# Kernel optimization log

Hardware: AMD Instinct MI355X
Metric: run time of the kernel (lower is better)

The kernel has to match this reference:

```python
import jax, jax.numpy as jnp
import numpy as np

FG_FRACTION = 0.5
BATCHSIZE = 256
NUM_IMAGES = 1
NUM_CLASSES = 21
FG_THRESH = 0.5
BG_THRESH_HI = 0.5
BG_THRESH_LO = 0.1
ROIS_PER_IMAGE = BATCHSIZE // NUM_IMAGES                      # 256
FG_ROIS_PER_IMAGE = int(round(FG_FRACTION * ROIS_PER_IMAGE))  # 128
BG_ROIS_PER_IMAGE = ROIS_PER_IMAGE - FG_ROIS_PER_IMAGE        # 128


def _make_boxes(key, n, img=1000.0, max_wh=200.0):
    k1, k2 = jax.random.split(key)
    xy = jax.random.uniform(k1, (n, 2), dtype=jnp.float32) * (img - max_wh)
    wh = jax.random.uniform(k2, (n, 2), dtype=jnp.float32) * max_wh + 1.0
    return jnp.concatenate([xy, xy + wh], axis=1)  # valid [x1,y1,x2,y2]


def setup_inputs() -> dict:
    key = jax.random.key(0)
    k1, k2, k3 = jax.random.split(key, 3)
    N, G = 250000, 128
    rois = _make_boxes(k1, N)
    all_rois = jnp.concatenate([jnp.zeros((N, 1), jnp.float32), rois], axis=1)  # [N,5], col0 = image idx
    gt_boxes = _make_boxes(k2, G)                                               # [G,4]
    gt_labels = jax.random.randint(k3, (G,), 1, NUM_CLASSES).astype(jnp.int32)  # fg classes 1..20
    return {"all_rois": all_rois, "gt_boxes": gt_boxes, "gt_labels": gt_labels}


def _iou(a, b):
    area_a = (a[:, 2] - a[:, 0] + 1.0) * (a[:, 3] - a[:, 1] + 1.0)
    area_b = (b[:, 2] - b[:, 0] + 1.0) * (b[:, 3] - b[:, 1] + 1.0)
    ix1 = jnp.maximum(a[:, None, 0], b[None, :, 0])
    iy1 = jnp.maximum(a[:, None, 1], b[None, :, 1])
    ix2 = jnp.minimum(a[:, None, 2], b[None, :, 2])
    iy2 = jnp.minimum(a[:, None, 3], b[None, :, 3])
    iw = jnp.clip(ix2 - ix1 + 1.0, 0.0)
    ih = jnp.clip(iy2 - iy1 + 1.0, 0.0)
    inter = iw * ih
    return inter / (area_a[:, None] + area_b[None, :] - inter)


def _bbox_transform(ex, gt):
    ew = ex[:, 2] - ex[:, 0] + 1.0
    eh = ex[:, 3] - ex[:, 1] + 1.0
    ecx = ex[:, 0] + 0.5 * ew
    ecy = ex[:, 1] + 0.5 * eh
    gw = gt[:, 2] - gt[:, 0] + 1.0
    gh = gt[:, 3] - gt[:, 1] + 1.0
    gcx = gt[:, 0] + 0.5 * gw
    gcy = gt[:, 1] + 0.5 * gh
    return jnp.stack([(gcx - ecx) / ew, (gcy - ecy) / eh,
                      jnp.log(gw / ew), jnp.log(gh / eh)], axis=1)


def _proposal_target(all_rois, gt_boxes, gt_labels):
    G = gt_boxes.shape[0]
    # append gt boxes (with image-index 0 column) to the proposal set
    gt_rois = jnp.concatenate([jnp.zeros((G, 1), all_rois.dtype), gt_boxes], axis=1)
    all_rois = jnp.concatenate([all_rois, gt_rois], axis=0)          # [N+G, 5]

    overlaps = _iou(all_rois[:, 1:5], gt_boxes)                       # [N+G, G] -- dominant memory traffic
    gt_assignment = jnp.argmax(overlaps, axis=1)                      # [N+G]
    max_ov = jnp.max(overlaps, axis=1)                                # [N+G]
    labels_all = gt_labels[gt_assignment]                             # [N+G]

    fg_mask = max_ov >= FG_THRESH
    bg_mask = (max_ov < BG_THRESH_HI) & (max_ov >= BG_THRESH_LO)

    # random fg/bg sampling: top-k over random keys restricted to each mask
    u = jax.random.uniform(jax.random.key(42), (all_rois.shape[0],), dtype=jnp.float32)
    fg_idx = jax.lax.top_k(jnp.where(fg_mask, u, -1.0), FG_ROIS_PER_IMAGE)[1]
    bg_idx = jax.lax.top_k(jnp.where(bg_mask, u, -1.0), BG_ROIS_PER_IMAGE)[1]
    keep = jnp.concatenate([fg_idx, bg_idx])                          # [256]

    valid_fg = fg_mask[fg_idx]  # if fewer fg than requested, pad slots get label 0
    labels = jnp.concatenate([jnp.where(valid_fg, labels_all[fg_idx], 0),
                              jnp.zeros((BG_ROIS_PER_IMAGE,), labels_all.dtype)])

    rois = all_rois[keep]                                             # [256, 5]
    targets = _bbox_transform(rois[:, 1:5], gt_boxes[gt_assignment[keep]])  # [256, 4]

    # scatter targets into class-specific columns [256, 4*num_classes]
    onehot = jax.nn.one_hot(labels, NUM_CLASSES, dtype=targets.dtype)
    bbox_targets = (onehot[:, :, None] * targets[:, None, :]).reshape(ROIS_PER_IMAGE, 4 * NUM_CLASSES)
    bbox_targets = bbox_targets * (labels > 0)[:, None].astype(targets.dtype)
    return rois, labels, bbox_targets


def reference(all_rois, gt_boxes, gt_labels):
    return _proposal_target(all_rois, gt_boxes, gt_labels)
```

## Files before the change

### kernel.cpp

```cpp
#include <hip/hip_runtime.h>
#include <stdint.h>

#define GMAX 128
#define TK 128
#define NBINS 4096
#define CAND_MAX 4096
#define NUM_CLASSES 21

typedef float f32x4u __attribute__((ext_vector_type(4), aligned(4)));

__device__ __forceinline__ void threefry2x32(uint32_t k0, uint32_t k1,
                                             uint32_t& x0, uint32_t& x1) {
  uint32_t ks0 = k0, ks1 = k1, ks2 = k0 ^ k1 ^ 0x1BD11BDAu;
  x0 += ks0; x1 += ks1;
#define TF_ROUND(r) { x0 += x1; x1 = (x1 << (r)) | (x1 >> (32 - (r))); x1 ^= x0; }
  TF_ROUND(13) TF_ROUND(15) TF_ROUND(26) TF_ROUND(6)
  x0 += ks1; x1 += ks2 + 1u;
  TF_ROUND(17) TF_ROUND(29) TF_ROUND(16) TF_ROUND(24)
  x0 += ks2; x1 += ks0 + 2u;
  TF_ROUND(13) TF_ROUND(15) TF_ROUND(26) TF_ROUND(6)
  x0 += ks0; x1 += ks1 + 3u;
  TF_ROUND(17) TF_ROUND(29) TF_ROUND(16) TF_ROUND(24)
  x0 += ks1; x1 += ks2 + 4u;
  TF_ROUND(13) TF_ROUND(15) TF_ROUND(26) TF_ROUND(6)
  x0 += ks2; x1 += ks0 + 5u;
#undef TF_ROUND
}

__global__ void __launch_bounds__(512)
score_kernel(const float* __restrict__ all_rois,
             const float* __restrict__ gt_boxes,
             uint32_t* __restrict__ score,
             uint32_t* __restrict__ hist,
             int* __restrict__ meta,
             int N, int M, int G) {
  __shared__ uint64_t lds_key[256];
  const int t = threadIdx.x;
  const int lane = t & 63;
  const int wave = t >> 6;
  const int wq = wave & 3;
  const int half = __builtin_amdgcn_readfirstlane(wave >> 2);
  const int i = blockIdx.x * 256 + wq * 64 + lane;
  const bool active = (i < M);

  float bx1 = 0.0f, by1 = 0.0f, bx2 = 0.0f, by2 = 0.0f;
  if (active) {
    if (i < N) {
      f32x4u v = *reinterpret_cast<const f32x4u*>(all_rois + (size_t)i * 5 + 1);
      bx1 = v.x; by1 = v.y; bx2 = v.z; by2 = v.w;
    } else {
      float4 b = reinterpret_cast<const float4*>(gt_boxes)[i - N];
      bx1 = b.x; by1 = b.y; bx2 = b.z; by2 = b.w;
    }
  }
  const float area = __fmul_rn(__fadd_rn(__fsub_rn(bx2, bx1), 1.0f),
                               __fadd_rn(__fsub_rn(by2, by1), 1.0f));
  float best = -1.0f;
  int bi = 0;
  const float4* __restrict__ gt4 = reinterpret_cast<const float4*>(gt_boxes);
  const int g0 = half * 64;
#pragma unroll 8
  for (int g = 0; g < 64; ++g) {
    const float4 gb = gt4[g0 + g];
    float ga = __fmul_rn(__fadd_rn(__fsub_rn(gb.z, gb.x), 1.0f),
                         __fadd_rn(__fsub_rn(gb.w, gb.y), 1.0f));
    float ix1 = fmaxf(bx1, gb.x);
    float iy1 = fmaxf(by1, gb.y);
    float ix2 = fminf(bx2, gb.z);
    float iy2 = fminf(by2, gb.w);
    float iw = fmaxf(__fadd_rn(__fsub_rn(ix2, ix1), 1.0f), 0.0f);
    float ih = fmaxf(__fadd_rn(__fsub_rn(iy2, iy1), 1.0f), 0.0f);
    float inter = __fmul_rn(iw, ih);
    float uni = __fsub_rn(__fadd_rn(area, ga), inter);
    float ov = __fdiv_rn(inter, uni);
    if (ov > best) { best = ov; bi = g0 + g; }
  }

  const uint64_t mykey = ((uint64_t)__float_as_uint(best) << 32) |
                         (uint64_t)(uint32_t)(127 - bi);
  if (half == 1) lds_key[wq * 64 + lane] = mykey;
  __syncthreads();

  if (half == 0) {
    uint64_t kk = lds_key[wq * 64 + lane];
    if (mykey > kk) kk = mykey;
    best = __uint_as_float((uint32_t)(kk >> 32));
    bi = 127 - (int)(kk & 127ull);

    if (active) {
      uint32_t cx0 = 0u, cx1 = (uint32_t)i;
      threefry2x32(0u, 42u, cx0, cx1);
      uint32_t ubits = (cx0 ^ cx1) >> 9;
      uint32_t fg = (best >= 0.5f) ? 1u : 0u;
      uint32_t bg = (!fg && best >= 0.1f) ? 1u : 0u;
      score[i] = (ubits << 9) | ((uint32_t)bi << 2) | (fg << 1) | bg;
      if (fg)      atomicAdd(&hist[ubits >> 11], 1u);
      else if (bg) atomicAdd(&hist[NBINS + (ubits >> 11)], 1u);
    }
  }

  asm volatile("s_waitcnt vmcnt(0)" ::: "memory");
  __syncthreads();
  __shared__ unsigned s_prev;
  if (t == 0) s_prev = atomicAdd((unsigned int*)&meta[2], 1u);
  __syncthreads();
  if (s_prev != gridDim.x - 1) return;

  __shared__ uint64_t gs[512];
  __shared__ int s_jstar[2];
  const int b0 = 8 * t;
  uint64_t acc = 0;
  for (int k = 0; k < 8; ++k) {
    uint32_t hf = __hip_atomic_load(&hist[b0 + k], __ATOMIC_RELAXED,
                                    __HIP_MEMORY_SCOPE_AGENT);
    uint32_t hb = __hip_atomic_load(&hist[NBINS + b0 + k], __ATOMIC_RELAXED,
                                    __HIP_MEMORY_SCOPE_AGENT);
    acc += ((uint64_t)hf << 32) | (uint64_t)hb;
  }
  gs[t] = acc;
  if (t < 2) s_jstar[t] = -1;
  __syncthreads();
  for (int d = 1; d < 512; d <<= 1) {
    uint64_t add = (t + d < 512) ? gs[t + d] : 0ull;
    __syncthreads();
    gs[t] += add;
    __syncthreads();
  }
  uint32_t vfg = (uint32_t)(gs[t] >> 32);
  uint32_t vbg = (uint32_t)gs[t];
  uint32_t nfg = (t < 511) ? (uint32_t)(gs[t + 1] >> 32) : 0u;
  uint32_t nbg = (t < 511) ? (uint32_t)gs[t + 1] : 0u;
  if (vfg >= (uint32_t)TK && (t == 511 || nfg < (uint32_t)TK)) s_jstar[0] = t;
  if (vbg >= (uint32_t)TK && (t == 511 || nbg < (uint32_t)TK)) s_jstar[1] = t;
  __syncthreads();
  if (t == 0) {
    for (int m = 0; m < 2; ++m) {
      int j = s_jstar[m], B = -1;
      if (j >= 0) {
        uint32_t base = 0;
        if (j < 511)
          base = (m == 0) ? (uint32_t)(gs[j + 1] >> 32) : (uint32_t)gs[j + 1];
        B = 8 * j;
        for (int b = 8 * j + 7; b >= 8 * j; --b) {
          base += __hip_atomic_load(&hist[m * NBINS + b], __ATOMIC_RELAXED,
                                    __HIP_MEMORY_SCOPE_AGENT);
          if (base >= (uint32_t)TK) { B = b; break; }
        }
      }
      meta[4 + m] = B;
    }
  }
}

__global__ void __launch_bounds__(256)
compact_final_kernel(const float* __restrict__ all_rois,
                     const float* __restrict__ gt_boxes,
                     const int* __restrict__ gt_labels,
                     const uint32_t* __restrict__ score, int M, int N,
                     int* __restrict__ meta,
                     uint64_t* __restrict__ cand_g,
                     float* __restrict__ out) {
  const int t = threadIdx.x;

  {
    const int bth[2] = {meta[4], meta[5]};
    const int base = (blockIdx.x * 256 + t) * 4;
    if (base < M) {
      uint32_t ss[4];
      int lim;
      if (base + 3 < M) {
        uint4 s4 = *reinterpret_cast<const uint4*>(score + base);
        ss[0] = s4.x; ss[1] = s4.y; ss[2] = s4.z; ss[3] = s4.w;
        lim = 4;
      } else {
        lim = M - base;
        for (int k = 0; k < lim; ++k) ss[k] = score[base + k];
      }
      for (int k = 0; k < lim; ++k) {
        uint32_t s = ss[k];
        uint32_t mb = s & 3u;
        if (!mb) continue;
        int m = (mb & 2u) ? 0 : 1;
        int B = bth[m];
        if (B >= 0 && (int)(s >> 20) < B) continue;
        int p = atomicAdd(&meta[m], 1);
        if (p < CAND_MAX)
          atomicExch((unsigned long long*)&cand_g[(size_t)m * CAND_MAX + p],
                     (((uint64_t)((s >> 9) + 1u)) << 32) |
                         (uint64_t)(~(uint32_t)(base + k)));
      }
    }
  }

  asm volatile("s_waitcnt vmcnt(0)" ::: "memory");
  __syncthreads();
  __shared__ unsigned s_prev;
  if (t == 0) s_prev = atomicAdd((unsigned int*)&meta[3], 1u);
  __syncthreads();
  if (s_prev != gridDim.x - 1) return;

  __shared__ uint64_t cand[CAND_MAX];
  __shared__ int keep[2 * TK];
  __shared__ int fgvalid[TK];
  __shared__ float s_tx[2 * TK], s_ty[2 * TK], s_tw[2 * TK], s_th[2 * TK];
  __shared__ int s_label[2 * TK];

  for (int m = 0; m < 2; ++m) {
    int cnt = (int)__hip_atomic_load((unsigned int*)&meta[m], __ATOMIC_RELAXED,
                                     __HIP_MEMORY_SCOPE_AGENT);
    if (cnt > CAND_MAX) cnt = CAND_MAX;
    for (int p = t; p < cnt; p += 256)
      cand[p] = __hip_atomic_load(
          (unsigned long long*)&cand_g[(size_t)m * CAND_MAX + p],
          __ATOMIC_RELAXED, __HIP_MEMORY_SCOPE_AGENT);
    __syncthreads();
    for (int p = t; p < cnt; p += 256) {
      uint64_t key = cand[p];
      int r = 0;
      for (int j = 0; j < cnt; ++j) r += (cand[j] > key) ? 1 : 0;
      if (r < TK) {
        keep[m * TK + r] = (int)(~(uint32_t)(key & 0xFFFFFFFFull));
        if (m == 0) fgvalid[r] = 1;
      }
    }
    __syncthreads();
    if (cnt < TK && t == 0) {
      int fill = cnt;
      uint32_t mask_bit = (m == 0) ? 2u : 1u;
      for (int i2 = 0; i2 < M && fill < TK; ++i2)
        if (!(score[i2] & mask_bit)) {
          keep[m * TK + fill] = i2;
          if (m == 0) fgvalid[fill] = 0;
          fill++;
        }
    }
    __syncthreads();
  }

  const int R = 2 * TK;
  float* rois_out   = out;
  float* labels_out = out + (size_t)R * 5;
  float* bt_out     = out + (size_t)R * 5 + R;

  {
    const int i = keep[t];
    float rimg, rx1, ry1, rx2, ry2;
    if (i < N) {
      rimg = all_rois[(size_t)i * 5 + 0];
      rx1  = all_rois[(size_t)i * 5 + 1];
      ry1  = all_rois[(size_t)i * 5 + 2];
      rx2  = all_rois[(size_t)i * 5 + 3];
      ry2  = all_rois[(size_t)i * 5 + 4];
    } else {
      int g = i - N;
      rimg = 0.0f;
      rx1 = gt_boxes[g * 4 + 0]; ry1 = gt_boxes[g * 4 + 1];
      rx2 = gt_boxes[g * 4 + 2]; ry2 = gt_boxes[g * 4 + 3];
    }
    rois_out[t * 5 + 0] = rimg;
    rois_out[t * 5 + 1] = rx1;
    rois_out[t * 5 + 2] = ry1;
    rois_out[t * 5 + 3] = rx2;
    rois_out[t * 5 + 4] = ry2;

    const int ga = (int)((score[i] >> 2) & 127u);
    int label = (t < TK && fgvalid[t]) ? gt_labels[ga] : 0;
    labels_out[t] = (float)label;
    s_label[t] = label;

    float gx1 = gt_boxes[ga * 4 + 0], gy1 = gt_boxes[ga * 4 + 1];
    float gx2 = gt_boxes[ga * 4 + 2], gy2 = gt_boxes[ga * 4 + 3];
    float ew = rx2 - rx1 + 1.0f, eh = ry2 - ry1 + 1.0f;
    float ecx = rx1 + 0.5f * ew, ecy = ry1 + 0.5f * eh;
    float gw = gx2 - gx1 + 1.0f, gh = gy2 - gy1 + 1.0f;
    float gcx = gx1 + 0.5f * gw, gcy = gy1 + 0.5f * gh;
    s_tx[t] = (gcx - ecx) / ew;
    s_ty[t] = (gcy - ecy) / eh;
    s_tw[t] = logf(gw / ew);
    s_th[t] = logf(gh / eh);
  }
  __syncthreads();

  const int TOT = R * 4 * NUM_CLASSES;
  for (int idx = t; idx < TOT; idx += 256) {
    int r = idx / (4 * NUM_CLASSES);
    int c = idx - r * (4 * NUM_CLASSES);
    int lab = s_label[r];
    float v = 0.0f;
    if (lab > 0 && (c >> 2) == lab) {
      int cc = c & 3;
      v = (cc == 0) ? s_tx[r] : (cc == 1) ? s_ty[r] : (cc == 2) ? s_tw[r] : s_th[r];
    }
    bt_out[idx] = v;
  }
}

extern "C" void kernel_launch(void* const* d_in, const int* in_sizes, int n_in,
                              void* d_out, int out_size, void* d_ws, size_t ws_size,
                              hipStream_t stream) {
  const float* all_rois = (const float*)d_in[0];
  const float* gt_boxes = (const float*)d_in[1];
  const int*   gt_labels = (const int*)d_in[2];
  const int N = in_sizes[0] / 5;
  const int G = in_sizes[2];
  const int M = N + G;

  char* ws = (char*)d_ws;
  int* meta = (int*)ws;
  uint32_t* hist = (uint32_t*)(ws + 256);
  size_t off = 256 + (size_t)2 * NBINS * 4;
  uint32_t* score = (uint32_t*)(ws + off);
  off += (((size_t)M * 4) + 255) & ~(size_t)255;
  uint64_t* cand = (uint64_t*)(ws + off);
  float* out = (float*)d_out;

  hipMemsetAsync(ws, 0, 256 + (size_t)2 * NBINS * 4, stream);
  const int nblocks = (M + 255) / 256;
  score_kernel<<<nblocks, 512, 0, stream>>>(all_rois, gt_boxes, score,
                                            hist, meta, N, M, G);
  const int nb4 = ((M + 3) / 4 + 255) / 256;
  compact_final_kernel<<<nb4, 256, 0, stream>>>(all_rois, gt_boxes, gt_labels,
                                                score, M, N, meta, cand, out);
}
```

Before: 122.1 us.

## Split compact and final stages into separate kernels; precompute GT areas in LDS

The fused compact_final kernel used a last-block-done atomic counter to elect one block for the final selection. That stage is now split into a compact kernel and a single-block 1024-thread final kernel, which removes the grid-wide atomic handshake and agent-scope atomic loads and stores. The final stage's rank sort and output writes now run with four times as many threads. Separately, the score kernel precomputes GT box areas into shared memory once per block, so the inner IoU loop no longer recomputes them, at the cost of one extra barrier. The trade is an extra kernel launch against the removed serialization.

Result: faster. 109.9 us (-9.9%).

```diff
diff --git a/kernel.cpp b/kernel.cpp
--- a/kernel.cpp
+++ b/kernel.cpp
@@ -35,6 +35,7 @@
              int* __restrict__ meta,
              int N, int M, int G) {
   __shared__ uint64_t lds_key[256];
+  __shared__ float sga[GMAX];
   const int t = threadIdx.x;
   const int lane = t & 63;
   const int wave = t >> 6;
@@ -43,27 +44,34 @@
   const int i = blockIdx.x * 256 + wq * 64 + lane;
   const bool active = (i < M);
 
+  const float4* __restrict__ gt4 = reinterpret_cast<const float4*>(gt_boxes);
+  if (t < GMAX) {
+    float4 b = gt4[t];
+    sga[t] = __fmul_rn(__fadd_rn(__fsub_rn(b.z, b.x), 1.0f),
+                       __fadd_rn(__fsub_rn(b.w, b.y), 1.0f));
+  }
+
   float bx1 = 0.0f, by1 = 0.0f, bx2 = 0.0f, by2 = 0.0f;
   if (active) {
     if (i < N) {
       f32x4u v = *reinterpret_cast<const f32x4u*>(all_rois + (size_t)i * 5 + 1);
       bx1 = v.x; by1 = v.y; bx2 = v.z; by2 = v.w;
     } else {
-      float4 b = reinterpret_cast<const float4*>(gt_boxes)[i - N];
+      float4 b = gt4[i - N];
       bx1 = b.x; by1 = b.y; bx2 = b.z; by2 = b.w;
     }
   }
   const float area = __fmul_rn(__fadd_rn(__fsub_rn(bx2, bx1), 1.0f),
                                __fadd_rn(__fsub_rn(by2, by1), 1.0f));
+  __syncthreads();
+
   float best = -1.0f;
   int bi = 0;
-  const float4* __restrict__ gt4 = reinterpret_cast<const float4*>(gt_boxes);
   const int g0 = half * 64;
 #pragma unroll 8
   for (int g = 0; g < 64; ++g) {
     const float4 gb = gt4[g0 + g];
-    float ga = __fmul_rn(__fadd_rn(__fsub_rn(gb.z, gb.x), 1.0f),
-                         __fadd_rn(__fsub_rn(gb.w, gb.y), 1.0f));
+    const float ga = sga[g0 + g];
     float ix1 = fmaxf(bx1, gb.x);
     float iy1 = fmaxf(by1, gb.y);
     float ix2 = fminf(bx2, gb.z);
@@ -153,68 +161,57 @@
 }
 
 __global__ void __launch_bounds__(256)
-compact_final_kernel(const float* __restrict__ all_rois,
-                     const float* __restrict__ gt_boxes,
-                     const int* __restrict__ gt_labels,
-                     const uint32_t* __restrict__ score, int M, int N,
-                     int* __restrict__ meta,
-                     uint64_t* __restrict__ cand_g,
-                     float* __restrict__ out) {
-  const int t = threadIdx.x;
-
-  {
-    const int bth[2] = {meta[4], meta[5]};
-    const int base = (blockIdx.x * 256 + t) * 4;
-    if (base < M) {
-      uint32_t ss[4];
-      int lim;
-      if (base + 3 < M) {
-        uint4 s4 = *reinterpret_cast<const uint4*>(score + base);
-        ss[0] = s4.x; ss[1] = s4.y; ss[2] = s4.z; ss[3] = s4.w;
-        lim = 4;
-      } else {
-        lim = M - base;
-        for (int k = 0; k < lim; ++k) ss[k] = score[base + k];
-      }
-      for (int k = 0; k < lim; ++k) {
-        uint32_t s = ss[k];
-        uint32_t mb = s & 3u;
-        if (!mb) continue;
-        int m = (mb & 2u) ? 0 : 1;
-        int B = bth[m];
-        if (B >= 0 && (int)(s >> 20) < B) continue;
-        int p = atomicAdd(&meta[m], 1);
-        if (p < CAND_MAX)
-          atomicExch((unsigned long long*)&cand_g[(size_t)m * CAND_MAX + p],
-                     (((uint64_t)((s >> 9) + 1u)) << 32) |
-                         (uint64_t)(~(uint32_t)(base + k)));
-      }
-    }
-  }
-
-  asm volatile("s_waitcnt vmcnt(0)" ::: "memory");
-  __syncthreads();
-  __shared__ unsigned s_prev;
-  if (t == 0) s_prev = atomicAdd((unsigned int*)&meta[3], 1u);
-  __syncthreads();
-  if (s_prev != gridDim.x - 1) return;
-
+compact_kernel(const uint32_t* __restrict__ score, int M,
+               int* __restrict__ meta,
+               uint64_t* __restrict__ cand) {
+  const int bth[2] = {meta[4], meta[5]};
+  const int base = (blockIdx.x * 256 + threadIdx.x) * 4;
+  if (base >= M) return;
+  uint32_t ss[4];
+  int lim;
+  if (base + 3 < M) {
+    uint4 s4 = *reinterpret_cast<const uint4*>(score + base);
+    ss[0] = s4.x; ss[1] = s4.y; ss[2] = s4.z; ss[3] = s4.w;
+    lim = 4;
+  } else {
+    lim = M - base;
+    for (int k = 0; k < lim; ++k) ss[k] = score[base + k];
+  }
+  for (int k = 0; k < lim; ++k) {
+    uint32_t s = ss[k];
+    uint32_t mb = s & 3u;
+    if (!mb) continue;
+    int m = (mb & 2u) ? 0 : 1;
+    int B = bth[m];
+    if (B >= 0 && (int)(s >> 20) < B) continue;
+    int p = atomicAdd(&meta[m], 1);
+    if (p < CAND_MAX)
+      cand[(size_t)m * CAND_MAX + p] =
+          (((uint64_t)((s >> 9) + 1u)) << 32) | (uint64_t)(~(uint32_t)(base + k));
+  }
+}
+
+__global__ void __launch_bounds__(1024)
+final_kernel(const float* __restrict__ all_rois,
+             const float* __restrict__ gt_boxes,
+             const int* __restrict__ gt_labels,
+             const uint32_t* __restrict__ score,
+             const uint64_t* __restrict__ cand_g,
+             const int* __restrict__ meta,
+             float* __restrict__ out, int N, int M) {
   __shared__ uint64_t cand[CAND_MAX];
   __shared__ int keep[2 * TK];
   __shared__ int fgvalid[TK];
   __shared__ float s_tx[2 * TK], s_ty[2 * TK], s_tw[2 * TK], s_th[2 * TK];
   __shared__ int s_label[2 * TK];
+  const int t = threadIdx.x;
 
   for (int m = 0; m < 2; ++m) {
-    int cnt = (int)__hip_atomic_load((unsigned int*)&meta[m], __ATOMIC_RELAXED,
-                                     __HIP_MEMORY_SCOPE_AGENT);
-    if (cnt > CAND_MAX) cnt = CAND_MAX;
-    for (int p = t; p < cnt; p += 256)
-      cand[p] = __hip_atomic_load(
-          (unsigned long long*)&cand_g[(size_t)m * CAND_MAX + p],
-          __ATOMIC_RELAXED, __HIP_MEMORY_SCOPE_AGENT);
-    __syncthreads();
-    for (int p = t; p < cnt; p += 256) {
+    int cnt = meta[m]; if (cnt > CAND_MAX) cnt = CAND_MAX;
+    for (int p = t; p < cnt; p += 1024)
+      cand[p] = cand_g[(size_t)m * CAND_MAX + p];
+    __syncthreads();
+    for (int p = t; p < cnt; p += 1024) {
       uint64_t key = cand[p];
       int r = 0;
       for (int j = 0; j < cnt; ++j) r += (cand[j] > key) ? 1 : 0;
@@ -242,7 +239,7 @@
   float* labels_out = out + (size_t)R * 5;
   float* bt_out     = out + (size_t)R * 5 + R;
 
-  {
+  if (t < R) {
     const int i = keep[t];
     float rimg, rx1, ry1, rx2, ry2;
     if (i < N) {
@@ -282,7 +279,7 @@
   __syncthreads();
 
   const int TOT = R * 4 * NUM_CLASSES;
-  for (int idx = t; idx < TOT; idx += 256) {
+  for (int idx = t; idx < TOT; idx += 1024) {
     int r = idx / (4 * NUM_CLASSES);
     int c = idx - r * (4 * NUM_CLASSES);
     int lab = s_label[r];
@@ -319,6 +316,7 @@
   score_kernel<<<nblocks, 512, 0, stream>>>(all_rois, gt_boxes, score,
                                             hist, meta, N, M, G);
   const int nb4 = ((M + 3) / 4 + 255) / 256;
-  compact_final_kernel<<<nb4, 256, 0, stream>>>(all_rois, gt_boxes, gt_labels,
-                                                score, M, N, meta, cand, out);
-}
+  compact_kernel<<<nb4, 256, 0, stream>>>(score, M, meta, cand);
+  final_kernel<<<1, 1024, 0, stream>>>(all_rois, gt_boxes, gt_labels, score,
+                                       cand, meta, out, N, M);
+}
```
